# Kernel tuning notes

Measured on AMD Instinct MI355X. Metric: run time of the kernel, lower is better.

The kernel has to match this reference:

```python
import jax, jax.numpy as jnp
import numpy as np
from jax import lax

NUM_CLASSES = 10
NUM_ITERS = 3


def conv2d(x, w, b, stride):
    # x: [B,C,H,W], w: [O,I,kh,kw]
    y = lax.conv_general_dilated(x, w, (stride, stride), 'VALID',
                                 dimension_numbers=('NCHW', 'OIHW', 'NCHW'))
    return y + b[None, :, None, None]


def squash(t, axis=-1):
    sn = jnp.sum(t * t, axis=axis, keepdims=True)
    return (sn / (1.0 + sn)) * t / jnp.sqrt(sn)


def routing(x, W, num_iters=NUM_ITERS):
    # x: [B,R,Ci], W: [C,R,Ci,Co] -> outputs [B,C,Co]
    # priors[c,b,r,o] = sum_i x[b,r,i] * W[c,r,i,o]
    priors = jnp.einsum('bri,crio->cbro', x, W)  # [C,B,R,Co]
    C, B, R, Co = priors.shape
    # torch logits are [C,B,R,1,Co] but identical along Co (zeros init,
    # delta broadcast), so a [C,B,R,1] logit is mathematically identical.
    logits = jnp.zeros((C, B, R, 1), priors.dtype)
    outputs = None
    for i in range(num_iters):
        probs = jax.nn.softmax(logits, axis=2)            # over route nodes
        s = jnp.sum(probs * priors, axis=2, keepdims=True)  # [C,B,1,Co]
        outputs = squash(s, axis=-1)
        if i != num_iters - 1:
            logits = logits + jnp.sum(priors * outputs, axis=-1, keepdims=True)
    return jnp.transpose(outputs[:, :, 0, :], (1, 0, 2))  # [B,C,Co]


def setup_inputs() -> dict:
    key = jax.random.key(0)
    ks = jax.random.split(key, 16)
    B = 32
    s = 0.05
    inp = {
        'x': jax.random.normal(ks[0], (B, 1, 61, 61), jnp.float32),
        'conv0_w': jax.random.normal(ks[1], (256, 1, 9, 9), jnp.float32) * s,
        'conv0_b': jnp.zeros((256,), jnp.float32),
        'conv1_w': jax.random.normal(ks[2], (256, 256, 9, 9), jnp.float32) * s,
        'conv1_b': jnp.zeros((256,), jnp.float32),
        # 8 primary-capsule convs stacked: [8*32, 256, 9, 9]
        'prim_w': jax.random.normal(ks[3], (8 * 32, 256, 9, 9), jnp.float32) * s,
        'prim_b': jnp.zeros((8 * 32,), jnp.float32),
        'W1': jax.random.normal(ks[4], (64, 32 * 6 * 6, 8, 16), jnp.float32) * s,
        'W2': jax.random.normal(ks[5], (NUM_CLASSES, 64, 16, 16), jnp.float32) * s,
        'dec_w1': jax.random.normal(ks[6], (16 * NUM_CLASSES, 1024), jnp.float32) * s,
        'dec_b1': jnp.zeros((1024,), jnp.float32),
        'dec_w2': jax.random.normal(ks[7], (1024, 2048), jnp.float32) * s,
        'dec_b2': jnp.zeros((2048,), jnp.float32),
        'dec_w3': jax.random.normal(ks[8], (2048, 4096), jnp.float32) * s,
        'dec_b3': jnp.zeros((4096,), jnp.float32),
    }
    return inp


def reference(x, conv0_w, conv0_b, conv1_w, conv1_b, prim_w, prim_b,
              W1, W2, dec_w1, dec_b1, dec_w2, dec_b2, dec_w3, dec_b3):
    B = x.shape[0]
    h = jax.nn.relu(conv2d(x, conv0_w, conv0_b, 2))       # [B,256,27,27]
    h = jax.nn.relu(conv2d(h, conv1_w, conv1_b, 1))       # [B,256,19,19]
    # primary capsules: 8 convs of 32 channels each, k9 s2 -> [B,256,6,6]
    p = conv2d(h, prim_w, prim_b, 2)
    # torch: each capsule conv -> view(B, 32*6*6, 1), cat on last -> [B,1152,8]
    p = p.reshape(B, 8, 32 * 6 * 6)                        # [B,8,1152]
    p = jnp.transpose(p, (0, 2, 1))                        # [B,1152,8]
    p = squash(p, axis=-1)
    u = routing(p, W1)                                     # [B,64,16]
    v = routing(u, W2)                                     # [B,10,16]
    classes = jnp.sqrt(jnp.sum(v * v, axis=-1))            # [B,10]
    classes = jax.nn.softmax(classes, axis=-1)
    y = jax.nn.one_hot(jnp.argmax(classes, axis=1), NUM_CLASSES,
                       dtype=v.dtype)                       # [B,10]
    y = lax.stop_gradient(y)
    z = (v * y[:, :, None]).reshape(B, -1)                 # [B,160]
    d = jax.nn.relu(z @ dec_w1 + dec_b1)
    d = jax.nn.relu(d @ dec_w2 + dec_b2)
    reconstructions = jax.nn.sigmoid(d @ dec_w3 + dec_b3)  # [B,4096]
    return classes, reconstructions
```

## Files before the change

### kernel.cpp

```cpp
#include <hip/hip_runtime.h>
#include <hip/hip_bf16.h>
#include <math.h>


#define NB 32

typedef _Float16 f16;
typedef f16 f16x2 __attribute__((ext_vector_type(2)));
typedef f16 f16x4 __attribute__((ext_vector_type(4)));
typedef f16 f16x8 __attribute__((ext_vector_type(8)));
typedef float f32x4 __attribute__((ext_vector_type(4)));

__device__ __forceinline__ int swz(int row, int q) {
  return row * 64 + ((q * 16) ^ (((row >> 1) & 3) << 4));
}

__global__ __launch_bounds__(256) void wprep_kernel(const float* __restrict__ w,
                                                    f16* __restrict__ wo) {
  int idx = blockIdx.x * 256 + threadIdx.x;
  int oc = idx >> 8, ic = idx & 255;
  const float* src = w + (size_t)(oc * 256 + ic) * 81;
  f16* dst = wo + oc * 256 + ic;
  for (int tap = 0; tap < 81; ++tap)
    dst[(size_t)tap * 65536] = (f16)src[tap];
}

__global__ __launch_bounds__(256) void conv0_kernel(
    const float* __restrict__ x, const float* __restrict__ w,
    const float* __restrict__ bias, f16* __restrict__ outf) {
  int b = blockIdx.x, ocg = blockIdx.y, z = blockIdx.z;
  __shared__ float img[61 * 61];
  __shared__ __align__(16) float wl[81][32];
  int t = threadIdx.x;
  for (int i = t; i < 61 * 61; i += 256) img[i] = x[b * 3721 + i];
  for (int i = t; i < 81 * 32; i += 256) {
    int k = i >> 5, oc = i & 31;
    wl[k][oc] = w[(ocg * 32 + oc) * 81 + k];
  }
  __syncthreads();
  int ocs = (t & 7) * 4;
  int pg  = t >> 3;
  int oc0 = ocg * 32 + ocs;
  float b0 = bias[oc0 + 0], b1 = bias[oc0 + 1], b2 = bias[oc0 + 2],
        b3 = bias[oc0 + 3];
  for (int p = pg + z * 32; p < 729; p += 64) {
    int oh = p / 27, ow = p - oh * 27;
    float a0 = 0.f, a1 = 0.f, a2 = 0.f, a3 = 0.f;
    const float* ib = &img[oh * 2 * 61 + ow * 2];
#pragma unroll
    for (int kh = 0; kh < 9; ++kh) {
#pragma unroll
      for (int kw = 0; kw < 9; ++kw) {
        float v = ib[kh * 61 + kw];
        const float4 wv =
            *reinterpret_cast<const float4*>(&wl[kh * 9 + kw][ocs]);
        a0 += v * wv.x; a1 += v * wv.y; a2 += v * wv.z; a3 += v * wv.w;
      }
    }
    int po = oh * 28 + ow;
    f16x4 hv;
    hv[0] = (f16)fmaxf(a0 + b0, 0.f);
    hv[1] = (f16)fmaxf(a1 + b1, 0.f);
    hv[2] = (f16)fmaxf(a2 + b2, 0.f);
    hv[3] = (f16)fmaxf(a3 + b3, 0.f);
    *(f16x4*)&outf[((size_t)b * 756 + po) * 256 + oc0] = hv;
  }
}

__global__ __launch_bounds__(256, 2) void conv1_mfma(
    const f16* __restrict__ xin,
    const f16* __restrict__ wA,
    f16* __restrict__ part) {
  int b = blockIdx.x, ocg = blockIdx.y, ksp = blockIdx.z;
  __shared__ __align__(16) f16 blds[784 * 32];
  int t = threadIdx.x;
  int w = t >> 6, lane = t & 63, kg = lane >> 4, ln = lane & 15;
  int prow[6];
#pragma unroll
  for (int nf = 0; nf < 6; ++nf) {
    int n = w * 96 + nf * 16 + ln;
    int oh = n / 20, ow = n - oh * 20;
    prow[nf] = oh * 28 + ow;
  }
  f32x4 acc[4][6];
#pragma unroll
  for (int m = 0; m < 4; ++m)
#pragma unroll
    for (int nf = 0; nf < 6; ++nf) acc[m][nf] = (f32x4){0.f, 0.f, 0.f, 0.f};

  const f16* xb = xin + (size_t)b * 756 * 256 + ksp * 64;
  const f16* abase = wA + (size_t)(ocg * 64 + ln) * 256 + ksp * 64 + kg * 8;
  for (int icc = 0; icc < 2; ++icc) {
    __syncthreads();
    for (int i = t; i < 3136; i += 256) {
      int p28 = i >> 2, q = i & 3;
      int p = (p28 < 756) ? p28 : (p28 - 28);
      f16x8 v = *(const f16x8*)(xb + (size_t)p * 256 + icc * 32 + q * 8);
      *(f16x8*)((char*)blds + swz(p28, q)) = v;
    }
    const f16* ap = abase + icc * 32;
    f16x8 aN[4];
#pragma unroll
    for (int m = 0; m < 4; ++m) aN[m] = *(const f16x8*)(ap + m * 4096);
    __syncthreads();
#pragma unroll 3
    for (int tap = 0; tap < 81; ++tap) {
      f16x8 aC[4];
#pragma unroll
      for (int m = 0; m < 4; ++m) aC[m] = aN[m];
      const f16* apn = ap + (size_t)(tap + 1) * 65536;
#pragma unroll
      for (int m = 0; m < 4; ++m) aN[m] = *(const f16x8*)(apn + m * 4096);
      int kh = tap / 9, kw = tap - kh * 9;
      int shift = kh * 28 + kw;
      f16x8 bf[6];
#pragma unroll
      for (int nf = 0; nf < 6; ++nf)
        bf[nf] = *(const f16x8*)((const char*)blds + swz(prow[nf] + shift, kg));
#pragma unroll
      for (int m = 0; m < 4; ++m)
#pragma unroll
        for (int nf = 0; nf < 6; ++nf)
          acc[m][nf] = __builtin_amdgcn_mfma_f32_16x16x32_f16(
              aC[m], bf[nf], acc[m][nf], 0, 0, 0);
    }
  }
  f16* pout = part + ((size_t)ksp * 32 + b) * 384 * 256 + ocg * 64;
#pragma unroll
  for (int m = 0; m < 4; ++m)
#pragma unroll
    for (int nf = 0; nf < 6; ++nf) {
      int n = w * 96 + nf * 16 + ln;
      int oc = m * 16 + kg * 4;
      f16x4 v;
#pragma unroll
      for (int j = 0; j < 4; ++j) v[j] = (f16)acc[m][nf][j];
      *(f16x4*)(pout + (size_t)n * 256 + oc) = v;
    }
}

__global__ void comb1_kernel(const f16* __restrict__ part,
                             const float* __restrict__ bias,
                             f16* __restrict__ h1f) {
  int idx = blockIdx.x * 256 + threadIdx.x;
  if (idx >= 32 * 380 * 32) return;
  int ocq = idx & 31, rem = idx >> 5;
  int p = rem % 380, b = rem / 380;
  float a[8];
#pragma unroll
  for (int j = 0; j < 8; ++j) a[j] = bias[ocq * 8 + j];
#pragma unroll
  for (int k = 0; k < 4; ++k) {
    f16x8 v = *(const f16x8*)&part[(((size_t)k * 32 + b) * 384 + p) * 256 +
                                   ocq * 8];
#pragma unroll
    for (int j = 0; j < 8; ++j) a[j] += (float)v[j];
  }
  f16x8 o;
#pragma unroll
  for (int j = 0; j < 8; ++j) o[j] = (f16)fmaxf(a[j], 0.f);
  *(f16x8*)&h1f[((size_t)b * 380 + p) * 256 + ocq * 8] = o;
}

__global__ __launch_bounds__(256, 2) void prim_mfma(
    const f16* __restrict__ xin,
    const f16* __restrict__ wB,
    float* __restrict__ part2) {
  int ip = blockIdx.x, ocg = blockIdx.y, ksp = blockIdx.z;
  __shared__ __align__(16) f16 blds[768 * 32];
  int t = threadIdx.x;
  int w = t >> 6, lane = t & 63, kg = lane >> 4, ln = lane & 15;
  int mg = w >> 1, ng = w & 1;
  int rbase[3];
#pragma unroll
  for (int nf = 0; nf < 3; ++nf) {
    int rem = nf * 16 + ln;
    int oh6 = rem >> 3, ow6 = rem & 7;
    rbase[nf] = ng * 384 + oh6 * 40 + ow6 * 2;
  }
  f32x4 acc[4][3];
#pragma unroll
  for (int m = 0; m < 4; ++m)
#pragma unroll
    for (int nf = 0; nf < 3; ++nf) acc[m][nf] = (f32x4){0.f, 0.f, 0.f, 0.f};

  for (int i = t; i < 3072; i += 256) {
    int pos = i >> 2, q = i & 3;
    int img = pos >= 384 ? 1 : 0;
    int p = pos - img * 384;
    if (p >= 380) p -= 20;
    f16x8 v = *(const f16x8*)(xin +
        ((size_t)(ip * 2 + img) * 380 + p) * 256 + ksp * 32 + q * 8);
    *(f16x8*)((char*)blds + swz(pos, q)) = v;
  }
  const f16* abase =
      wB + (size_t)(ocg * 128 + mg * 64 + ln) * 256 + ksp * 32 + kg * 8;
  f16x8 aN[4];
#pragma unroll
  for (int m = 0; m < 4; ++m) aN[m] = *(const f16x8*)(abase + m * 4096);
  __syncthreads();
#pragma unroll 3
  for (int tap = 0; tap < 81; ++tap) {
    f16x8 aC[4];
#pragma unroll
    for (int m = 0; m < 4; ++m) aC[m] = aN[m];
    const f16* apn = abase + (size_t)(tap + 1) * 65536;
#pragma unroll
    for (int m = 0; m < 4; ++m) aN[m] = *(const f16x8*)(apn + m * 4096);
    int kh = tap / 9, kw = tap - kh * 9;
    int shift = kh * 20 + kw;
    f16x8 bf[3];
#pragma unroll
    for (int nf = 0; nf < 3; ++nf)
      bf[nf] = *(const f16x8*)((const char*)blds + swz(rbase[nf] + shift, kg));
#pragma unroll
    for (int m = 0; m < 4; ++m)
#pragma unroll
      for (int nf = 0; nf < 3; ++nf)
        acc[m][nf] = __builtin_amdgcn_mfma_f32_16x16x32_f16(
            aC[m], bf[nf], acc[m][nf], 0, 0, 0);
  }
  float* pout = part2 + ((size_t)ksp * 16 + ip) * 96 * 256 + ocg * 128;
#pragma unroll
  for (int m = 0; m < 4; ++m)
#pragma unroll
    for (int nf = 0; nf < 3; ++nf) {
      int n = ng * 48 + nf * 16 + ln;
      int oc = (mg * 4 + m) * 16 + kg * 4;
      *(f32x4*)(pout + (size_t)n * 256 + oc) = acc[m][nf];
    }
}

__global__ void comb2_kernel(const float* __restrict__ part2,
                             float* __restrict__ sum2) {
  int idx = blockIdx.x * 256 + threadIdx.x;
  if (idx >= 16 * 96 * 256) return;
  float a = 0.f;
#pragma unroll
  for (int k = 0; k < 8; ++k) a += part2[(size_t)k * 393216 + idx];
  sum2[idx] = a;
}

__global__ void prim_squash_kernel(const float* __restrict__ sum2,
                                   const float* __restrict__ bias,
                                   float* __restrict__ caps) {
  int idx = blockIdx.x * blockDim.x + threadIdx.x;
  if (idx >= NB * 1152) return;
  int b = idx / 1152, r = idx - b * 1152;
  int m = r / 36, s = r - m * 36;
  int oh6 = s / 6, ow6 = s - oh6 * 6;
  int n = (b & 1) * 48 + oh6 * 8 + ow6;
  const float* src = sum2 + ((size_t)(b >> 1) * 96 + n) * 256;
  float tv[8];
  float sn = 0.f;
#pragma unroll
  for (int g = 0; g < 8; ++g) {
    float v = src[g * 32 + m] + bias[g * 32 + m];
    tv[g] = v;
    sn += v * v;
  }
  float sc = sqrtf(sn) / (1.f + sn);
#pragma unroll
  for (int g = 0; g < 8; ++g) caps[idx * 8 + g] = tv[g] * sc;
}

__global__ __launch_bounds__(256) void priors1_kernel(
    const float* __restrict__ x,
    const float* __restrict__ W,
    f16* __restrict__ pri) {
  int c = blockIdx.x, rt = blockIdx.y;
  int r0 = rt * 32;
  __shared__ __align__(16) float xl[32 * 32 * 8];
  int t = threadIdx.x;
  for (int q = t; q < 2048; q += 256) {
    int b = q >> 6, j = q & 63;
    *(float4*)&xl[b * 256 + j * 4] =
        *(const float4*)&x[(size_t)b * 9216 + r0 * 8 + j * 4];
  }
  int rl = t >> 3, oq = t & 7;
  float w0[8], w1[8];
#pragma unroll
  for (int i = 0; i < 8; ++i) {
    const float2 wv = *(const float2*)&W[
        (((size_t)c * 1152 + r0 + rl) * 8 + i) * 16 + 2 * oq];
    w0[i] = wv.x; w1[i] = wv.y;
  }
  __syncthreads();
  f16* pout = pri + (size_t)c * 32 * 18432 + (r0 + rl) * 16 + 2 * oq;
#pragma unroll 4
  for (int b = 0; b < 32; ++b) {
    const float4 x0 = *(const float4*)&xl[b * 256 + rl * 8];
    const float4 x1 = *(const float4*)&xl[b * 256 + rl * 8 + 4];
    float s0 = x0.x * w0[0] + x0.y * w0[1] + x0.z * w0[2] + x0.w * w0[3] +
               x1.x * w0[4] + x1.y * w0[5] + x1.z * w0[6] + x1.w * w0[7];
    float s1 = x0.x * w1[0] + x0.y * w1[1] + x0.z * w1[2] + x0.w * w1[3] +
               x1.x * w1[4] + x1.y * w1[5] + x1.z * w1[6] + x1.w * w1[7];
    f16x2 hv; hv[0] = (f16)s0; hv[1] = (f16)s1;
    *(f16x2*)(pout + (size_t)b * 18432) = hv;
  }
}

__global__ __launch_bounds__(512) void route1_kernel(
    const f16* __restrict__ pri,
    float* __restrict__ out) {
  constexpr int R = 1152;
  constexpr int NREG = 36;
  int c = blockIdx.x, b = blockIdx.y;
  __shared__ float lg[R], pr[R];
  __shared__ float redA[8], redB[8];
  __shared__ float sred[8][16];
  __shared__ float vsh[17];
  int t    = threadIdx.x;
  int o    = t & 15;
  int rhi  = t >> 4;
  int wid  = t >> 6;
  int lane = t & 63;
  const f16* pb = pri + ((size_t)c * 32 + b) * (R * 16);

  float prireg[NREG];
#pragma unroll
  for (int k = 0; k < NREG; ++k)
    prireg[k] = (float)pb[(k * 32 + rhi) * 16 + o];
  for (int r = t; r < R; r += 512) lg[r] = 0.f;
  __syncthreads();

  for (int it = 0; it < 3; ++it) {
    float lm = -1e30f;
    for (int r = t; r < R; r += 512) lm = fmaxf(lm, lg[r]);
#pragma unroll
    for (int s2 = 1; s2 <= 32; s2 <<= 1) lm = fmaxf(lm, __shfl_xor(lm, s2));
    if (lane == 0) redA[wid] = lm;
    __syncthreads();
    if (t == 0) {
      float m8 = redA[0];
#pragma unroll
      for (int w = 1; w < 8; ++w) m8 = fmaxf(m8, redA[w]);
      redA[0] = m8;
    }
    __syncthreads();
    float m = redA[0];
    float ls = 0.f;
    for (int r = t; r < R; r += 512) {
      float e = __expf(lg[r] - m);
      pr[r] = e;
      ls += e;
    }
#pragma unroll
    for (int s2 = 1; s2 <= 32; s2 <<= 1) ls += __shfl_xor(ls, s2);
    if (lane == 0) redB[wid] = ls;
    __syncthreads();
    if (t == 0) {
      float s8 = 0.f;
#pragma unroll
      for (int w = 0; w < 8; ++w) s8 += redB[w];
      redB[0] = s8;
    }
    __syncthreads();
    float denom = redB[0];
    float part = 0.f;
#pragma unroll
    for (int k = 0; k < NREG; ++k) part += pr[k * 32 + rhi] * prireg[k];
    part += __shfl_xor(part, 16);
    part += __shfl_xor(part, 32);
    if (lane < 16) sred[wid][lane] = part;
    __syncthreads();
    if (t < 16) {
      float sv = 0.f;
#pragma unroll
      for (int w = 0; w < 8; ++w) sv += sred[w][t];
      vsh[t] = sv / denom;
    }
    __syncthreads();
    if (t == 0) {
      float sn = 0.f;
#pragma unroll
      for (int oo = 0; oo < 16; ++oo) sn += vsh[oo] * vsh[oo];
      vsh[16] = sqrtf(sn) / (1.f + sn);
    }
    __syncthreads();
    if (it < 2) {
      float vo = vsh[o] * vsh[16];
#pragma unroll
      for (int k = 0; k < NREG; ++k) {
        float val = prireg[k] * vo;
        val += __shfl_xor(val, 1);
        val += __shfl_xor(val, 2);
        val += __shfl_xor(val, 4);
        val += __shfl_xor(val, 8);
        if (o == 0) lg[k * 32 + rhi] += val;
      }
      __syncthreads();
    }
  }
  if (t < 16) out[((size_t)b * 64 + c) * 16 + t] = vsh[t] * vsh[16];
}

template <int R, int CI>
__global__ __launch_bounds__(512) void routing_kernel(
    const float* __restrict__ x,
    const float* __restrict__ W,
    float* __restrict__ out) {
  constexpr int NREG = R * 16 / 512;
  int c = blockIdx.x, b = blockIdx.y;
  int C = gridDim.x;
  __shared__ float xls[R * CI];
  extern __shared__ float rdyn[];
  float* lg = rdyn;
  float* pr = rdyn + R;
  __shared__ float redA[8], redB[8];
  __shared__ float sred[8][16];
  __shared__ float vsh[17];
  int t    = threadIdx.x;
  int o    = t & 15;
  int rhi  = t >> 4;
  int wid  = t >> 6;
  int lane = t & 63;
  const float* xb = x + (size_t)b * R * CI;
  const float* Wc = W + (size_t)c * R * CI * 16;

  for (int i = t; i < R * CI; i += 512) xls[i] = xb[i];
  for (int r = t; r < R; r += 512) lg[r] = 0.f;
  __syncthreads();

  float pri[NREG];
#pragma unroll
  for (int k = 0; k < NREG; ++k) {
    int r = k * 32 + rhi;
    float s = 0.f;
#pragma unroll
    for (int i = 0; i < CI; ++i)
      s += xls[r * CI + i] * Wc[((size_t)r * CI + i) * 16 + o];
    pri[k] = s;
  }

  for (int it = 0; it < 3; ++it) {
    float lm = -1e30f;
    for (int r = t; r < R; r += 512) lm = fmaxf(lm, lg[r]);
#pragma unroll
    for (int s2 = 1; s2 <= 32; s2 <<= 1) lm = fmaxf(lm, __shfl_xor(lm, s2));
    if (lane == 0) redA[wid] = lm;
    __syncthreads();
    if (t == 0) {
      float m8 = redA[0];
#pragma unroll
      for (int w = 1; w < 8; ++w) m8 = fmaxf(m8, redA[w]);
      redA[0] = m8;
    }
    __syncthreads();
    float m = redA[0];
    float ls = 0.f;
    for (int r = t; r < R; r += 512) {
      float e = __expf(lg[r] - m);
      pr[r] = e;
      ls += e;
    }
#pragma unroll
    for (int s2 = 1; s2 <= 32; s2 <<= 1) ls += __shfl_xor(ls, s2);
    if (lane == 0) redB[wid] = ls;
    __syncthreads();
    if (t == 0) {
      float s8 = 0.f;
#pragma unroll
      for (int w = 0; w < 8; ++w) s8 += redB[w];
      redB[0] = s8;
    }
    __syncthreads();
    float denom = redB[0];
    float part = 0.f;
#pragma unroll
    for (int k = 0; k < NREG; ++k) part += pr[k * 32 + rhi] * pri[k];
    part += __shfl_xor(part, 16);
    part += __shfl_xor(part, 32);
    if (lane < 16) sred[wid][lane] = part;
    __syncthreads();
    if (t < 16) {
      float sv = 0.f;
#pragma unroll
      for (int w = 0; w < 8; ++w) sv += sred[w][t];
      vsh[t] = sv / denom;
    }
    __syncthreads();
    if (t == 0) {
      float sn = 0.f;
#pragma unroll
      for (int oo = 0; oo < 16; ++oo) sn += vsh[oo] * vsh[oo];
      vsh[16] = sqrtf(sn) / (1.f + sn);
    }
    __syncthreads();
    if (it < 2) {
      float vo = vsh[o] * vsh[16];
#pragma unroll
      for (int k = 0; k < NREG; ++k) {
        float val = pri[k] * vo;
        val += __shfl_xor(val, 1);
        val += __shfl_xor(val, 2);
        val += __shfl_xor(val, 4);
        val += __shfl_xor(val, 8);
        if (o == 0) lg[k * 32 + rhi] += val;
      }
      __syncthreads();
    }
  }
  if (t < 16) out[((size_t)b * C + c) * 16 + t] = vsh[t] * vsh[16];
}

__global__ void classes_kernel(const float* __restrict__ v,
                               float* __restrict__ outc,
                               int* __restrict__ amaxb) {
  int b = blockIdx.x;
  int t = threadIdx.x;
  __shared__ float nrm[10];
  if (t < 10) {
    float sn = 0.f;
#pragma unroll
    for (int o = 0; o < 16; ++o) {
      float xv = v[(b * 10 + t) * 16 + o];
      sn += xv * xv;
    }
    nrm[t] = sqrtf(sn);
  }
  __syncthreads();
  if (t == 0) {
    float m = nrm[0];
    int am = 0;
    for (int c = 1; c < 10; ++c)
      if (nrm[c] > m) { m = nrm[c]; am = c; }
    float s = 0.f;
    float e[10];
    for (int c = 0; c < 10; ++c) { e[c] = __expf(nrm[c] - m); s += e[c]; }
    for (int c = 0; c < 10; ++c) outc[b * 10 + c] = e[c] / s;
    amaxb[b] = am;
  }
}

__global__ __launch_bounds__(256) void fc1s_kernel(
    const float* __restrict__ v, const int* __restrict__ amaxb,
    const float* __restrict__ w, const float* __restrict__ bias,
    float* __restrict__ out) {
  int n  = blockIdx.x * 256 + threadIdx.x;
  int b0 = blockIdx.y * 8;
  __shared__ float vls[8][16];
  __shared__ int ams[8];
  int t = threadIdx.x;
  if (t < 8) ams[t] = amaxb[b0 + t];
  __syncthreads();
  if (t < 128) {
    int bb = t >> 4, oo = t & 15;
    vls[bb][oo] = v[((b0 + bb) * 10 + ams[bb]) * 16 + oo];
  }
  __syncthreads();
  float bv = bias[n];
#pragma unroll
  for (int bb = 0; bb < 8; ++bb) {
    int row0 = ams[bb] * 16;
    float acc = bv;
#pragma unroll
    for (int oo = 0; oo < 16; ++oo)
      acc += vls[bb][oo] * w[(size_t)(row0 + oo) * 1024 + n];
    out[(size_t)(b0 + bb) * 1024 + n] = fmaxf(acc, 0.f);
  }
}

template <int K, int KCH>
__global__ __launch_bounds__(256) void fcsplit_kernel(
    const float* __restrict__ in, const float* __restrict__ w,
    float* __restrict__ pbuf, int N) {
  int n  = blockIdx.x * 256 + threadIdx.x;
  int b0 = blockIdx.y * 8;
  int k0 = blockIdx.z * KCH;
  __shared__ __align__(16) float inl[KCH * 8];
  for (int idx = threadIdx.x; idx < 8 * KCH; idx += 256) {
    int bb = idx / KCH, k = idx - bb * KCH;
    inl[k * 8 + bb] = in[(size_t)(b0 + bb) * K + k0 + k];
  }
  __syncthreads();
  float acc[8];
#pragma unroll
  for (int bb = 0; bb < 8; ++bb) acc[bb] = 0.f;
  for (int k = 0; k < KCH; ++k) {
    float wv = w[(size_t)(k0 + k) * N + n];
    const float4 i0 = *reinterpret_cast<const float4*>(&inl[k * 8]);
    const float4 i1 = *reinterpret_cast<const float4*>(&inl[k * 8 + 4]);
    acc[0] += i0.x * wv; acc[1] += i0.y * wv;
    acc[2] += i0.z * wv; acc[3] += i0.w * wv;
    acc[4] += i1.x * wv; acc[5] += i1.y * wv;
    acc[6] += i1.z * wv; acc[7] += i1.w * wv;
  }
#pragma unroll
  for (int bb = 0; bb < 8; ++bb)
    pbuf[((size_t)blockIdx.z * 32 + b0 + bb) * N + n] = acc[bb];
}

template <int KS, bool RELU, bool SIG>
__global__ void fccomb_kernel(const float* __restrict__ pbuf,
                              const float* __restrict__ bias,
                              float* __restrict__ out, int N) {
  int idx = blockIdx.x * 256 + threadIdx.x;
  if (idx >= 32 * N) return;
  int b = idx / N, n = idx - b * N;
  float a = bias[n];
#pragma unroll
  for (int kz = 0; kz < KS; ++kz) a += pbuf[((size_t)kz * 32 + b) * N + n];
  if (RELU) a = fmaxf(a, 0.f);
  if (SIG)  a = 1.f / (1.f + __expf(-a));
  out[idx] = a;
}

extern "C" void kernel_launch(void* const* d_in, const int* in_sizes, int n_in,
                              void* d_out, int out_size, void* d_ws,
                              size_t ws_size, hipStream_t stream) {
  const float* x       = (const float*)d_in[0];
  const float* conv0_w = (const float*)d_in[1];
  const float* conv0_b = (const float*)d_in[2];
  const float* conv1_w = (const float*)d_in[3];
  const float* conv1_b = (const float*)d_in[4];
  const float* prim_w  = (const float*)d_in[5];
  const float* prim_b  = (const float*)d_in[6];
  const float* W1      = (const float*)d_in[7];
  const float* W2      = (const float*)d_in[8];
  const float* dec_w1  = (const float*)d_in[9];
  const float* dec_b1  = (const float*)d_in[10];
  const float* dec_w2  = (const float*)d_in[11];
  const float* dec_b2  = (const float*)d_in[12];
  const float* dec_w3  = (const float*)d_in[13];
  const float* dec_b3  = (const float*)d_in[14];
  float* out = (float*)d_out;

  float* ws    = (float*)d_ws;
  float* caps  = ws;
  float* u     = caps + 294912;
  float* vc    = u + 32768;
  int*   amaxb = (int*)(vc + 5120);
  float* trans = vc + 5120 + 32;

  f16* wA    = (f16*)trans;
  f16* wB    = wA + 5308416;
  f16* h0f   = wB + 5308416;
  f16* h1f   = h0f + 6193152;
  f16* part1 = h1f + 3112960;
  float* part2 = (float*)part1;
  float* sum2  = part2 + 3145728;
  f16* pri1  = (f16*)trans;
  float* d1  = trans;
  float* d2  = d1 + 32768;
  float* pb2 = d2 + 65536;
  float* pb3 = pb2 + 262144;

  wprep_kernel<<<256, 256, 0, stream>>>(conv1_w, wA);
  wprep_kernel<<<256, 256, 0, stream>>>(prim_w, wB);

  conv0_kernel<<<dim3(NB, 8, 2), 256, 0, stream>>>(x, conv0_w, conv0_b, h0f);

  conv1_mfma<<<dim3(NB, 4, 4), 256, 0, stream>>>(h0f, wA, part1);
  comb1_kernel<<<1520, 256, 0, stream>>>(part1, conv1_b, h1f);

  prim_mfma<<<dim3(16, 2, 8), 256, 0, stream>>>(h1f, wB, part2);
  comb2_kernel<<<1536, 256, 0, stream>>>(part2, sum2);

  prim_squash_kernel<<<(NB * 1152 + 255) / 256, 256, 0, stream>>>(sum2, prim_b,
                                                                  caps);

  priors1_kernel<<<dim3(64, 36), 256, 0, stream>>>(caps, W1, pri1);
  route1_kernel<<<dim3(64, NB), 512, 0, stream>>>(pri1, u);

  routing_kernel<64, 16>
      <<<dim3(10, NB), 512, 2 * 64 * sizeof(float), stream>>>(u, W2, vc);

  classes_kernel<<<NB, 64, 0, stream>>>(vc, out, amaxb);

  fc1s_kernel<<<dim3(4, 4), 256, 0, stream>>>(vc, amaxb, dec_w1, dec_b1, d1);

  fcsplit_kernel<1024, 256>
      <<<dim3(8, 4, 4), 256, 0, stream>>>(d1, dec_w2, pb2, 2048);
  fccomb_kernel<4, true, false>
      <<<256, 256, 0, stream>>>(pb2, dec_b2, d2, 2048);

  fcsplit_kernel<2048, 256>
      <<<dim3(16, 4, 8), 256, 0, stream>>>(d2, dec_w3, pb3, 4096);
  fccomb_kernel<8, false, true>
      <<<512, 256, 0, stream>>>(pb3, dec_b3, out + 320, 4096);
}
```

Measured before the change: 484.7 us.

## Stage conv weight tiles through double-buffered LDS instead of per-wave global loads

In conv1_mfma and prim_mfma, the A (weight) fragments were previously loaded directly from global memory by every wave, with redundant loads across waves. Now each block cooperatively loads the per-tap weight tile once into a double-buffered LDS array and the waves read their fragments from LDS. This removes duplicate global traffic for weights. The cost is a __syncthreads per tap, extra LDS reads and more LDS use per block, which could reduce occupancy. The global-to-LDS prefetch of the next tap no longer overlaps as freely with the MFMAs.

```diff
diff --git a/kernel.cpp b/kernel.cpp
--- a/kernel.cpp
+++ b/kernel.cpp
@@ -73,8 +73,10 @@
     f16* __restrict__ part) {
   int b = blockIdx.x, ocg = blockIdx.y, ksp = blockIdx.z;
   __shared__ __align__(16) f16 blds[784 * 32];
+  __shared__ __align__(16) f16 alds[2][64 * 32];
   int t = threadIdx.x;
   int w = t >> 6, lane = t & 63, kg = lane >> 4, ln = lane & 15;
+  int aoc = t >> 2, aq = t & 3;
   int prow[6];
 #pragma unroll
   for (int nf = 0; nf < 6; ++nf) {
@@ -89,7 +91,7 @@
     for (int nf = 0; nf < 6; ++nf) acc[m][nf] = (f32x4){0.f, 0.f, 0.f, 0.f};
 
   const f16* xb = xin + (size_t)b * 756 * 256 + ksp * 64;
-  const f16* abase = wA + (size_t)(ocg * 64 + ln) * 256 + ksp * 64 + kg * 8;
+  const f16* ab = wA + (size_t)(ocg * 64 + aoc) * 256 + ksp * 64 + aq * 8;
   for (int icc = 0; icc < 2; ++icc) {
     __syncthreads();
     for (int i = t; i < 3136; i += 256) {
@@ -98,21 +100,23 @@
       f16x8 v = *(const f16x8*)(xb + (size_t)p * 256 + icc * 32 + q * 8);
       *(f16x8*)((char*)blds + swz(p28, q)) = v;
     }
-    const f16* ap = abase + icc * 32;
-    f16x8 aN[4];
-#pragma unroll
-    for (int m = 0; m < 4; ++m) aN[m] = *(const f16x8*)(ap + m * 4096);
-    __syncthreads();
-#pragma unroll 3
+    {
+      f16x8 v = *(const f16x8*)(ab + icc * 32);
+      *(f16x8*)((char*)alds[0] + swz(aoc, aq)) = v;
+    }
+    __syncthreads();
     for (int tap = 0; tap < 81; ++tap) {
-      f16x8 aC[4];
-#pragma unroll
-      for (int m = 0; m < 4; ++m) aC[m] = aN[m];
-      const f16* apn = ap + (size_t)(tap + 1) * 65536;
-#pragma unroll
-      for (int m = 0; m < 4; ++m) aN[m] = *(const f16x8*)(apn + m * 4096);
+      int cur = tap & 1;
+      if (tap < 80) {
+        f16x8 v = *(const f16x8*)(ab + (size_t)(tap + 1) * 65536 + icc * 32);
+        *(f16x8*)((char*)alds[cur ^ 1] + swz(aoc, aq)) = v;
+      }
       int kh = tap / 9, kw = tap - kh * 9;
       int shift = kh * 28 + kw;
+      f16x8 af[4];
+#pragma unroll
+      for (int m = 0; m < 4; ++m)
+        af[m] = *(const f16x8*)((const char*)alds[cur] + swz(m * 16 + ln, kg));
       f16x8 bf[6];
 #pragma unroll
       for (int nf = 0; nf < 6; ++nf)
@@ -122,7 +126,8 @@
 #pragma unroll
         for (int nf = 0; nf < 6; ++nf)
           acc[m][nf] = __builtin_amdgcn_mfma_f32_16x16x32_f16(
-              aC[m], bf[nf], acc[m][nf], 0, 0, 0);
+              af[m], bf[nf], acc[m][nf], 0, 0, 0);
+      __syncthreads();
     }
   }
   f16* pout = part + ((size_t)ksp * 32 + b) * 384 * 256 + ocg * 64;
@@ -168,6 +173,7 @@
     float* __restrict__ part2) {
   int ip = blockIdx.x, ocg = blockIdx.y, ksp = blockIdx.z;
   __shared__ __align__(16) f16 blds[768 * 32];
+  __shared__ __align__(16) f16 alds[2][128 * 32];
   int t = threadIdx.x;
   int w = t >> 6, lane = t & 63, kg = lane >> 4, ln = lane & 15;
   int mg = w >> 1, ng = w & 1;
@@ -193,22 +199,32 @@
         ((size_t)(ip * 2 + img) * 380 + p) * 256 + ksp * 32 + q * 8);
     *(f16x8*)((char*)blds + swz(pos, q)) = v;
   }
-  const f16* abase =
-      wB + (size_t)(ocg * 128 + mg * 64 + ln) * 256 + ksp * 32 + kg * 8;
-  f16x8 aN[4];
-#pragma unroll
-  for (int m = 0; m < 4; ++m) aN[m] = *(const f16x8*)(abase + m * 4096);
-  __syncthreads();
-#pragma unroll 3
+  const f16* ab = wB + (size_t)(ocg * 128) * 256 + ksp * 32;
+#pragma unroll
+  for (int i = t; i < 512; i += 256) {
+    int oc = i >> 2, q = i & 3;
+    f16x8 v = *(const f16x8*)(ab + (size_t)oc * 256 + q * 8);
+    *(f16x8*)((char*)alds[0] + swz(oc, q)) = v;
+  }
+  __syncthreads();
   for (int tap = 0; tap < 81; ++tap) {
-    f16x8 aC[4];
-#pragma unroll
-    for (int m = 0; m < 4; ++m) aC[m] = aN[m];
-    const f16* apn = abase + (size_t)(tap + 1) * 65536;
-#pragma unroll
-    for (int m = 0; m < 4; ++m) aN[m] = *(const f16x8*)(apn + m * 4096);
+    int cur = tap & 1;
+    if (tap < 80) {
+#pragma unroll
+      for (int i = t; i < 512; i += 256) {
+        int oc = i >> 2, q = i & 3;
+        f16x8 v = *(const f16x8*)(ab + (size_t)(tap + 1) * 65536 +
+                                  (size_t)oc * 256 + q * 8);
+        *(f16x8*)((char*)alds[cur ^ 1] + swz(oc, q)) = v;
+      }
+    }
     int kh = tap / 9, kw = tap - kh * 9;
     int shift = kh * 20 + kw;
+    f16x8 af[4];
+#pragma unroll
+    for (int m = 0; m < 4; ++m)
+      af[m] = *(const f16x8*)((const char*)alds[cur] +
+                              swz((mg * 4 + m) * 16 + ln, kg));
     f16x8 bf[3];
 #pragma unroll
     for (int nf = 0; nf < 3; ++nf)
@@ -218,7 +234,8 @@
 #pragma unroll
       for (int nf = 0; nf < 3; ++nf)
         acc[m][nf] = __builtin_amdgcn_mfma_f32_16x16x32_f16(
-            aC[m], bf[nf], acc[m][nf], 0, 0, 0);
+            af[m], bf[nf], acc[m][nf], 0, 0, 0);
+    __syncthreads();
   }
   float* pout = part2 + ((size_t)ksp * 16 + ip) * 96 * 256 + ocg * 128;
 #pragma unroll
```

Measured after the change: 459.5 us. 1.05x faster.
